# Kernel optimization log

Measured on AMD Instinct MI355X. Metric: run time of the kernel, lower is better.

The kernel has to match this reference:

```python
import jax, jax.numpy as jnp
import numpy as np

EPS = 1e-5
NUM_GROUPS = 32
NUM_HEADS = 4


def setup_inputs() -> dict:
    key = jax.random.key(0)
    ks = jax.random.split(key, 3)
    B, C, H, W = 4, 256, 64, 64
    x = jax.random.normal(ks[0], (B, C, H, W), dtype=jnp.float32)
    gn_w = jnp.ones((C,), jnp.float32)
    gn_b = jnp.zeros((C,), jnp.float32)
    qkv_w = jax.random.normal(ks[1], (3 * C, C), dtype=jnp.float32) * (C ** -0.5)
    qkv_b = jnp.zeros((3 * C,), jnp.float32)
    proj_w = jax.random.normal(ks[2], (C, C), dtype=jnp.float32) * (C ** -0.5)
    proj_b = jnp.zeros((C,), jnp.float32)
    return {"x": x, "gn_w": gn_w, "gn_b": gn_b, "qkv_w": qkv_w,
            "qkv_b": qkv_b, "proj_w": proj_w, "proj_b": proj_b}


def _group_norm(x, w, b):
    B, C, H, W = x.shape
    xg = x.reshape(B, NUM_GROUPS, C // NUM_GROUPS, H, W)
    mean = xg.mean(axis=(2, 3, 4), keepdims=True)
    var = xg.var(axis=(2, 3, 4), keepdims=True)
    xn = ((xg - mean) * jax.lax.rsqrt(var + EPS)).reshape(B, C, H, W)
    return xn * w[None, :, None, None] + b[None, :, None, None]


def reference(x, gn_w, gn_b, qkv_w, qkv_b, proj_w, proj_b):
    B, C, H, W = x.shape
    nh = NUM_HEADS
    d = C // nh
    L = H * W
    h = _group_norm(x, gn_w, gn_b)
    # 1x1 conv == channel matmul
    qkv = jnp.einsum('oc,bchw->bohw', qkv_w, h) + qkv_b[None, :, None, None]
    q, k, v = jnp.split(qkv, 3, axis=1)
    # (B, C, H, W) -> (B, nh, L, d)
    def to_heads(t):
        return t.reshape(B, nh, d, L).transpose(0, 1, 3, 2)
    q, k, v = to_heads(q), to_heads(k), to_heads(v)
    scale = d ** -0.5
    attn = jax.nn.softmax(jnp.einsum('bhqd,bhkd->bhqk', q, k) * scale, axis=-1)
    o = jnp.einsum('bhqk,bhkd->bhqd', attn, v)          # (B, nh, L, d)
    o = o.transpose(0, 1, 3, 2).reshape(B, C, H, W)
    o = jnp.einsum('oc,bchw->bohw', proj_w, o) + proj_b[None, :, None, None]
    return x + o
```

## Files before the change

kernel.cpp:

```cpp
#include <hip/hip_runtime.h>

#define B_   4
#define C_   256
#define L_   4096
#define NH_  4
#define D_   64
#define G_   32
#define CPG_ 8

typedef __bf16 bf16x8 __attribute__((ext_vector_type(8)));
typedef float  f32x4  __attribute__((ext_vector_type(4)));

__device__ __forceinline__ ushort f2bf(float f) {
  union { float f; unsigned u; } c; c.f = f;
  unsigned u = c.u;
  return (ushort)((u + 0x7fffu + ((u >> 16) & 1u)) >> 16);
}
__device__ __forceinline__ float bf2f(ushort h) {
  union { unsigned u; float f; } c; c.u = ((unsigned)h) << 16; return c.f;
}
__device__ __forceinline__ unsigned fbits(float f) {
  union { float f; unsigned u; } c; c.f = f; return c.u;
}
__device__ __forceinline__ float fastexp2(float x) {
#if __has_builtin(__builtin_amdgcn_exp2f)
  return __builtin_amdgcn_exp2f(x);
#else
  return exp2f(x);
#endif
}

__global__ __launch_bounds__(256) void cvt_kernel(const float* __restrict__ wq,
                                                  const float* __restrict__ wp,
                                                  ushort* __restrict__ oq,
                                                  ushort* __restrict__ op,
                                                  float* __restrict__ stats) {
  int t = blockIdx.x * 256 + threadIdx.x;
  if (blockIdx.x == 0) stats[threadIdx.x] = 0.f;
  const int NQ4 = (768 * 256) / 4;
  float4 v;
  if (t < NQ4) {
    v = ((const float4*)wq)[t];
    ((ushort4*)oq)[t] = make_ushort4(f2bf(v.x), f2bf(v.y), f2bf(v.z), f2bf(v.w));
  } else {
    int i = t - NQ4;
    v = ((const float4*)wp)[i];
    ((ushort4*)op)[i] = make_ushort4(f2bf(v.x), f2bf(v.y), f2bf(v.z), f2bf(v.w));
  }
}

__global__ __launch_bounds__(256) void gn_stats(const float* __restrict__ x,
                                                float* __restrict__ stats) {
  int bg = blockIdx.x >> 3, chunk = blockIdx.x & 7;
  int b = bg >> 5, g = bg & 31;
  const float* xg = x + ((size_t)b * C_ + g * CPG_) * L_ + chunk * 512;
  int tid = threadIdx.x;

  float s = 0.f, ss = 0.f;
  for (int c = 0; c < CPG_; ++c) {
    float2 v = ((const float2*)(xg + (size_t)c * L_))[tid];
    s  += v.x + v.y;
    ss += v.x * v.x + v.y * v.y;
  }
  for (int off = 32; off; off >>= 1) { s += __shfl_xor(s, off); ss += __shfl_xor(ss, off); }
  __shared__ float red[8];
  int w = tid >> 6;
  if ((tid & 63) == 0) { red[w] = s; red[4 + w] = ss; }
  __syncthreads();
  if (tid == 0) {
    atomicAdd(&stats[bg * 2],     red[0] + red[1] + red[2] + red[3]);
    atomicAdd(&stats[bg * 2 + 1], red[4] + red[5] + red[6] + red[7]);
  }
}

__global__ __launch_bounds__(256) void gn_apply(const float* __restrict__ x,
                                                const float* __restrict__ gw,
                                                const float* __restrict__ gb,
                                                const float* __restrict__ stats,
                                                ushort* __restrict__ hT) {
  int bg = blockIdx.x >> 3, chunk = blockIdx.x & 7;
  int b = bg >> 5, g = bg & 31;
  const float* xg = x + ((size_t)b * C_ + g * CPG_) * L_;
  int tid = threadIdx.x;

  const float inv_n = 1.0f / (CPG_ * L_);
  float mean = stats[bg * 2] * inv_n;
  float var  = stats[bg * 2 + 1] * inv_n - mean * mean;
  float rstd = rsqrtf(var + 1e-5f);

  float wv[CPG_], bv[CPG_];
  for (int c = 0; c < CPG_; ++c) { wv[c] = gw[g * CPG_ + c]; bv[c] = gb[g * CPG_ + c]; }

  for (int li = 0; li < 2; ++li) {
    int l = chunk * 512 + li * 256 + tid;
    union { ushort s[8]; uint4 u; } o;
    for (int c = 0; c < CPG_; ++c) {
      float v = xg[(size_t)c * L_ + l];
      o.s[c] = f2bf((v - mean) * rstd * wv[c] + bv[c]);
    }
    *(uint4*)(hT + ((size_t)b * L_ + l) * C_ + g * CPG_) = o.u;
  }
}

__global__ __launch_bounds__(256) void qkv_kernel(const ushort* __restrict__ hT,
                                                  const ushort* __restrict__ w,
                                                  const float* __restrict__ bias,
                                                  ushort* __restrict__ q,
                                                  ushort* __restrict__ k,
                                                  ushort* __restrict__ v) {
  int wid  = blockIdx.x * 4 + (threadIdx.x >> 6);
  int lane = threadIdx.x & 63;
  int quad = lane >> 4, col = lane & 15;
  int ot   = wid % 12;
  int rest = wid / 12;
  int lt   = rest & 127;
  int b    = rest >> 7;
  int o0 = ot * 64, l0 = lt * 32;

  const ushort* abase = w  + (size_t)(o0 + col) * C_ + quad * 8;
  const ushort* bbase = hT + ((size_t)b * L_ + l0 + col) * C_ + quad * 8;

  f32x4 acc[4][2];
  for (int i = 0; i < 4; ++i) for (int j = 0; j < 2; ++j)
    acc[i][j] = (f32x4){0.f, 0.f, 0.f, 0.f};

#pragma unroll
  for (int k0 = 0; k0 < C_; k0 += 32) {
    bf16x8 a[4], bb[2];
#pragma unroll
    for (int i = 0; i < 4; ++i) a[i]  = *(const bf16x8*)(abase + (size_t)(i * 16) * C_ + k0);
#pragma unroll
    for (int j = 0; j < 2; ++j) bb[j] = *(const bf16x8*)(bbase + (size_t)(j * 16) * C_ + k0);
#pragma unroll
    for (int i = 0; i < 4; ++i)
#pragma unroll
      for (int j = 0; j < 2; ++j)
        acc[i][j] = __builtin_amdgcn_mfma_f32_16x16x32_bf16(a[i], bb[j], acc[i][j], 0, 0, 0);
  }

  int third = o0 >> 8;
  int hh    = (o0 & 255) >> 6;
  float scale = (third == 0) ? 0.180336880111120f : 1.0f;
#pragma unroll
  for (int i = 0; i < 4; ++i) {
    int oo = o0 + i * 16 + quad * 4;
    int dd = i * 16 + quad * 4;
#pragma unroll
    for (int j = 0; j < 2; ++j) {
      int l = l0 + j * 16 + col;
      ushort pk[4];
      for (int r = 0; r < 4; ++r) pk[r] = f2bf((acc[i][j][r] + bias[oo + r]) * scale);
      if (third < 2) {
        ushort* dst = (third ? k : q) + (((size_t)(b * NH_ + hh) * L_ + l) * D_ + dd);
        *(ushort4*)dst = make_ushort4(pk[0], pk[1], pk[2], pk[3]);
      } else {
        for (int r = 0; r < 4; ++r)
          v[((size_t)(b * NH_ + hh) * D_ + dd + r) * L_ + l] = pk[r];
      }
    }
  }
}

__global__ __launch_bounds__(128, 2) void attn_kernel(const ushort* __restrict__ q,
                                                      const ushort* __restrict__ k,
                                                      const ushort* __restrict__ v,
                                                      ushort* __restrict__ p0,
                                                      ushort* __restrict__ p1,
                                                      float* __restrict__ psumbuf) {
  __shared__ __align__(16) ushort k_lds[2][64][72];
  __shared__ __align__(16) ushort v_lds[2][64][72];

  int tid   = threadIdx.x;
  int w     = tid >> 6, lane = tid & 63;
  int quad  = lane >> 4, col = lane & 15;
  int bid   = (int)blockIdx.x;
  bid = (bid & 7) * 128 + (bid >> 3);
  int split = bid >> 9;
  int bh    = (bid >> 5) & 15;
  int qblk  = bid & 31;

  const ushort* qp = q + (size_t)bh * L_ * D_;
  const ushort* kp = k + (size_t)bh * L_ * D_;
  const ushort* vp = v + (size_t)bh * D_ * L_;

  int qrow0 = qblk * 128 + w * 64;
  bf16x8 bq[4][2];
#pragma unroll
  for (int f = 0; f < 4; ++f)
#pragma unroll
    for (int c = 0; c < 2; ++c)
      bq[f][c] = *(const bf16x8*)(qp + (size_t)(qrow0 + f * 16 + col) * D_ + c * 32 + quad * 8);

  f32x4 oacc[4][4];
#pragma unroll
  for (int f = 0; f < 4; ++f)
    for (int t = 0; t < 4; ++t) oacc[f][t] = (f32x4){0.f, 0.f, 0.f, 0.f};
  float psum[4] = {0.f, 0.f, 0.f, 0.f};
  const f32x4 Z = (f32x4){0.f, 0.f, 0.f, 0.f};

  int vrow = tid >> 1, vhalf = tid & 1;
  int kt0 = split * (L_ / 2), kt_end = kt0 + L_ / 2;

#define STAGE_K(NB, A0, A1, A2, A3) { \
    *(uint4*)&k_lds[NB][(tid >> 3)][(tid & 7) * 8]      = A0; \
    *(uint4*)&k_lds[NB][16 + (tid >> 3)][(tid & 7) * 8] = A1; \
    *(uint4*)&k_lds[NB][32 + (tid >> 3)][(tid & 7) * 8] = A2; \
    *(uint4*)&k_lds[NB][48 + (tid >> 3)][(tid & 7) * 8] = A3; \
  }
#define STAGE_V(NB, C0, C1, C2, C3) { \
    ushort* vb_ = &v_lds[NB][vrow][vhalf * 32]; \
    *(uint2*)(vb_ + 0)  = make_uint2(C0.x, C0.y); \
    *(uint2*)(vb_ + 8)  = make_uint2(C0.z, C0.w); \
    *(uint2*)(vb_ + 16) = make_uint2(C1.x, C1.y); \
    *(uint2*)(vb_ + 24) = make_uint2(C1.z, C1.w); \
    *(uint2*)(vb_ + 4)  = make_uint2(C2.x, C2.y); \
    *(uint2*)(vb_ + 12) = make_uint2(C2.z, C2.w); \
    *(uint2*)(vb_ + 20) = make_uint2(C3.x, C3.y); \
    *(uint2*)(vb_ + 28) = make_uint2(C3.z, C3.w); \
  }

  {
    const uint4* ksrc = (const uint4*)(kp + (size_t)kt0 * D_);
    uint4 a0 = ksrc[tid], a1 = ksrc[tid + 128], a2 = ksrc[tid + 256], a3 = ksrc[tid + 384];
    const uint4* vsrc = (const uint4*)(vp + (size_t)vrow * L_ + kt0);
    uint4 c0 = vsrc[vhalf * 4], c1 = vsrc[vhalf * 4 + 1];
    uint4 c2 = vsrc[vhalf * 4 + 2], c3 = vsrc[vhalf * 4 + 3];
    STAGE_K(0, a0, a1, a2, a3);
    STAGE_V(0, c0, c1, c2, c3);
  }
  __syncthreads();

  int cur = 0;
  for (int kt = kt0; kt < kt_end; kt += 64) {
    bool has_next = (kt + 64) < kt_end;

    f32x4 s[2][4][2];
#pragma unroll
    for (int h = 0; h < 2; ++h) {
      bf16x8 a00 = *(const bf16x8*)&k_lds[cur][h * 32 + col][quad * 8];
      bf16x8 a01 = *(const bf16x8*)&k_lds[cur][h * 32 + col][32 + quad * 8];
      bf16x8 a10 = *(const bf16x8*)&k_lds[cur][h * 32 + 16 + col][quad * 8];
      bf16x8 a11 = *(const bf16x8*)&k_lds[cur][h * 32 + 16 + col][32 + quad * 8];
#pragma unroll
      for (int f = 0; f < 4; ++f) {
        s[h][f][0] = __builtin_amdgcn_mfma_f32_16x16x32_bf16(a00, bq[f][0], Z, 0, 0, 0);
        s[h][f][1] = __builtin_amdgcn_mfma_f32_16x16x32_bf16(a10, bq[f][0], Z, 0, 0, 0);
        s[h][f][0] = __builtin_amdgcn_mfma_f32_16x16x32_bf16(a01, bq[f][1], s[h][f][0], 0, 0, 0);
        s[h][f][1] = __builtin_amdgcn_mfma_f32_16x16x32_bf16(a11, bq[f][1], s[h][f][1], 0, 0, 0);
      }
    }

    uint4 nk0, nk1, nk2, nk3, nv0, nv1, nv2, nv3;
    if (has_next) {
      const uint4* ksrc = (const uint4*)(kp + (size_t)(kt + 64) * D_);
      nk0 = ksrc[tid]; nk1 = ksrc[tid + 128]; nk2 = ksrc[tid + 256]; nk3 = ksrc[tid + 384];
      const uint4* vsrc = (const uint4*)(vp + (size_t)vrow * L_ + (kt + 64));
      nv0 = vsrc[vhalf * 4];     nv1 = vsrc[vhalf * 4 + 1];
      nv2 = vsrc[vhalf * 4 + 2]; nv3 = vsrc[vhalf * 4 + 3];
    }

#pragma unroll
    for (int h = 0; h < 2; ++h) {
      bf16x8 pb[4];
#pragma unroll
      for (int f = 0; f < 4; ++f) {
        float pe0[4], pe1[4];
#pragma unroll
        for (int r = 0; r < 4; ++r) {
          pe0[r] = fastexp2(s[h][f][0][r]);
          pe1[r] = fastexp2(s[h][f][1][r]);
        }
        psum[f] += ((pe0[0] + pe0[1]) + (pe0[2] + pe0[3])) +
                   ((pe1[0] + pe1[1]) + (pe1[2] + pe1[3]));
        union { unsigned u[4]; bf16x8 v8; } pc;
        pc.u[0] = __builtin_amdgcn_perm(fbits(pe0[1]), fbits(pe0[0]), 0x07060302u);
        pc.u[1] = __builtin_amdgcn_perm(fbits(pe0[3]), fbits(pe0[2]), 0x07060302u);
        pc.u[2] = __builtin_amdgcn_perm(fbits(pe1[1]), fbits(pe1[0]), 0x07060302u);
        pc.u[3] = __builtin_amdgcn_perm(fbits(pe1[3]), fbits(pe1[2]), 0x07060302u);
        pb[f] = pc.v8;
      }
#pragma unroll
      for (int t = 0; t < 4; ++t) {
        bf16x8 av = *(const bf16x8*)&v_lds[cur][t * 16 + col][h * 32 + quad * 8];
#pragma unroll
        for (int f = 0; f < 4; ++f)
          oacc[f][t] = __builtin_amdgcn_mfma_f32_16x16x32_bf16(av, pb[f], oacc[f][t], 0, 0, 0);
      }
    }

    if (has_next) {
      int nb = cur ^ 1;
      STAGE_K(nb, nk0, nk1, nk2, nk3);
      STAGE_V(nb, nv0, nv1, nv2, nv3);
      __syncthreads();
      cur = nb;
    }
  }
#undef STAGE_K
#undef STAGE_V

  ushort* po = split ? p1 : p0;
#pragma unroll
  for (int f = 0; f < 4; ++f) {
    psum[f] += __shfl_xor(psum[f], 16);
    psum[f] += __shfl_xor(psum[f], 32);
    for (int t = 0; t < 4; ++t) {
      ushort ok[4];
      for (int r = 0; r < 4; ++r) ok[r] = f2bf(oacc[f][t][r]);
      ushort* dst = po + ((size_t)bh * L_ + qrow0 + f * 16 + col) * D_ + t * 16 + quad * 4;
      *(ushort4*)dst = make_ushort4(ok[0], ok[1], ok[2], ok[3]);
    }
    if (quad == 0)
      psumbuf[split * (16 * L_) + bh * L_ + qrow0 + f * 16 + col] = psum[f];
  }
}

__global__ __launch_bounds__(256) void comb_kernel(ushort* __restrict__ p0,
                                                   const ushort* __restrict__ p1,
                                                   const float* __restrict__ ps) {
  int idx = blockIdx.x * 256 + threadIdx.x;
  int row = idx >> 4;
  float inv = 1.0f / (ps[row] + ps[16 * L_ + row]);
  ushort4 a = ((const ushort4*)p0)[idx];
  ushort4 b = ((const ushort4*)p1)[idx];
  ((ushort4*)p0)[idx] = make_ushort4(
      f2bf((bf2f(a.x) + bf2f(b.x)) * inv),
      f2bf((bf2f(a.y) + bf2f(b.y)) * inv),
      f2bf((bf2f(a.z) + bf2f(b.z)) * inv),
      f2bf((bf2f(a.w) + bf2f(b.w)) * inv));
}

__global__ __launch_bounds__(256) void proj_kernel(const ushort* __restrict__ oin,
                                                   const ushort* __restrict__ pw,
                                                   const float* __restrict__ pb,
                                                   const float* __restrict__ x,
                                                   float* __restrict__ out) {
  int wid  = blockIdx.x * 4 + (threadIdx.x >> 6);
  int lane = threadIdx.x & 63;
  int quad = lane >> 4, col = lane & 15;
  int oct  = wid & 7;
  int rest = wid >> 3;
  int lt   = rest & 127;
  int b    = rest >> 7;
  int l0 = lt * 32, oc0 = oct * 32;

  f32x4 acc[2][2];
  for (int i = 0; i < 2; ++i) for (int j = 0; j < 2; ++j)
    acc[i][j] = (f32x4){0.f, 0.f, 0.f, 0.f};

#pragma unroll
  for (int k0 = 0; k0 < C_; k0 += 32) {
    int hh = k0 >> 6, dk = k0 & 63;
    bf16x8 a[2], bb[2];
#pragma unroll
    for (int i = 0; i < 2; ++i)
      a[i] = *(const bf16x8*)(oin + ((size_t)(b * NH_ + hh) * L_ + l0 + i * 16 + col) * D_ + dk + quad * 8);
#pragma unroll
    for (int j = 0; j < 2; ++j)
      bb[j] = *(const bf16x8*)(pw + (size_t)(oc0 + j * 16 + col) * C_ + k0 + quad * 8);
#pragma unroll
    for (int i = 0; i < 2; ++i)
#pragma unroll
      for (int j = 0; j < 2; ++j)
        acc[i][j] = __builtin_amdgcn_mfma_f32_16x16x32_bf16(a[i], bb[j], acc[i][j], 0, 0, 0);
  }

#pragma unroll
  for (int j = 0; j < 2; ++j) {
    int oc = oc0 + j * 16 + col;
    float bias = pb[oc];
#pragma unroll
    for (int i = 0; i < 2; ++i) {
      int l = l0 + i * 16 + quad * 4;
      size_t off = ((size_t)b * C_ + oc) * L_ + l;
      float4 xv = *(const float4*)(x + off);
      float4 ov = make_float4(acc[i][j][0] + bias + xv.x,
                              acc[i][j][1] + bias + xv.y,
                              acc[i][j][2] + bias + xv.z,
                              acc[i][j][3] + bias + xv.w);
      *(float4*)(out + off) = ov;
    }
  }
}

extern "C" void kernel_launch(void* const* d_in, const int* in_sizes, int n_in,
                              void* d_out, int out_size, void* d_ws, size_t ws_size,
                              hipStream_t stream) {
  const float* x      = (const float*)d_in[0];
  const float* gn_w   = (const float*)d_in[1];
  const float* gn_b   = (const float*)d_in[2];
  const float* qkv_w  = (const float*)d_in[3];
  const float* qkv_b  = (const float*)d_in[4];
  const float* proj_w = (const float*)d_in[5];
  const float* proj_b = (const float*)d_in[6];
  float* out = (float*)d_out;

  const size_t TEN = (size_t)B_ * C_ * L_;
  ushort* ws  = (ushort*)d_ws;
  ushort* q   = ws;
  ushort* k   = ws + TEN;
  ushort* v   = ws + 2 * TEN;
  ushort* oat = ws + 3 * TEN;
  ushort* wq  = ws + 4 * TEN;
  ushort* wp  = wq + 768 * 256;
  float*  stats = (float*)(wp + 256 * 256);
  ushort* hT  = (ushort*)d_out;
  ushort* p1  = (ushort*)d_out + TEN;
  float*  psb = (float*)d_out;

  cvt_kernel <<<256,       256, 0, stream>>>(qkv_w, proj_w, wq, wp, stats);
  gn_stats   <<<1024,      256, 0, stream>>>(x, stats);
  gn_apply   <<<1024,      256, 0, stream>>>(x, gn_w, gn_b, stats, hT);
  qkv_kernel <<<6144 / 4,  256, 0, stream>>>(hT, wq, qkv_b, q, k, v);
  attn_kernel<<<1024,      128, 0, stream>>>(q, k, v, oat, p1, psb);
  comb_kernel<<<4096,      256, 0, stream>>>(oat, p1, psb);
  proj_kernel<<<4096 / 4,  256, 0, stream>>>(oat, wp, proj_b, x, out);
}
```

Measured before the change: 224.4 us.

## Halve attention query tile, load V directly from global, swizzle K LDS

The attention kernel now gives each block 64 query rows instead of 128 (32 per wave), which doubles the grid to 2048 blocks and raises the launch-bounds occupancy hint from 2 to 3. V is no longer staged in shared memory: each wave reads its V fragments straight from global memory inside the loop. K uses an unpadded 64-wide LDS tile with an XOR swizzle to avoid bank conflicts, and the next K tile's prefetch is issued before the QK MFMAs. The goal is higher occupancy and less LDS traffic. The trade-off is that each block reuses K/V across half as many queries, so global and L2 traffic for K and V roughly doubles, and the V loads are narrow 8-byte accesses that sit in the critical path.

```diff
diff --git a/kernel.cpp b/kernel.cpp
--- a/kernel.cpp
+++ b/kernel.cpp
@@ -161,72 +161,60 @@
   }
 }
 
-__global__ __launch_bounds__(128, 2) void attn_kernel(const ushort* __restrict__ q,
+__global__ __launch_bounds__(128, 3) void attn_kernel(const ushort* __restrict__ q,
                                                       const ushort* __restrict__ k,
                                                       const ushort* __restrict__ v,
                                                       ushort* __restrict__ p0,
                                                       ushort* __restrict__ p1,
                                                       float* __restrict__ psumbuf) {
-  __shared__ __align__(16) ushort k_lds[2][64][72];
-  __shared__ __align__(16) ushort v_lds[2][64][72];
+  __shared__ __align__(16) ushort k_lds[2][64][64];
 
   int tid   = threadIdx.x;
   int w     = tid >> 6, lane = tid & 63;
   int quad  = lane >> 4, col = lane & 15;
   int bid   = (int)blockIdx.x;
-  bid = (bid & 7) * 128 + (bid >> 3);
-  int split = bid >> 9;
-  int bh    = (bid >> 5) & 15;
-  int qblk  = bid & 31;
+  bid = (bid & 7) * 256 + (bid >> 3);
+  int split = bid >> 10;
+  int bh    = (bid >> 6) & 15;
+  int qblk  = bid & 63;
 
   const ushort* qp = q + (size_t)bh * L_ * D_;
   const ushort* kp = k + (size_t)bh * L_ * D_;
   const ushort* vp = v + (size_t)bh * D_ * L_;
 
-  int qrow0 = qblk * 128 + w * 64;
-  bf16x8 bq[4][2];
-#pragma unroll
-  for (int f = 0; f < 4; ++f)
+  int qrow0 = qblk * 64 + w * 32;
+  bf16x8 bq[2][2];
+#pragma unroll
+  for (int f = 0; f < 2; ++f)
 #pragma unroll
     for (int c = 0; c < 2; ++c)
       bq[f][c] = *(const bf16x8*)(qp + (size_t)(qrow0 + f * 16 + col) * D_ + c * 32 + quad * 8);
 
-  f32x4 oacc[4][4];
-#pragma unroll
-  for (int f = 0; f < 4; ++f)
+  f32x4 oacc[2][4];
+#pragma unroll
+  for (int f = 0; f < 2; ++f)
     for (int t = 0; t < 4; ++t) oacc[f][t] = (f32x4){0.f, 0.f, 0.f, 0.f};
-  float psum[4] = {0.f, 0.f, 0.f, 0.f};
+  float psum[2] = {0.f, 0.f};
   const f32x4 Z = (f32x4){0.f, 0.f, 0.f, 0.f};
 
-  int vrow = tid >> 1, vhalf = tid & 1;
+  int wrow = tid >> 3;
+  int winn = ((tid & 7) ^ (wrow & 7)) * 8;
+  int sw0 = ((quad)     ^ (col & 7)) * 8;
+  int sw4 = ((quad + 4) ^ (col & 7)) * 8;
+
   int kt0 = split * (L_ / 2), kt_end = kt0 + L_ / 2;
 
 #define STAGE_K(NB, A0, A1, A2, A3) { \
-    *(uint4*)&k_lds[NB][(tid >> 3)][(tid & 7) * 8]      = A0; \
-    *(uint4*)&k_lds[NB][16 + (tid >> 3)][(tid & 7) * 8] = A1; \
-    *(uint4*)&k_lds[NB][32 + (tid >> 3)][(tid & 7) * 8] = A2; \
-    *(uint4*)&k_lds[NB][48 + (tid >> 3)][(tid & 7) * 8] = A3; \
-  }
-#define STAGE_V(NB, C0, C1, C2, C3) { \
-    ushort* vb_ = &v_lds[NB][vrow][vhalf * 32]; \
-    *(uint2*)(vb_ + 0)  = make_uint2(C0.x, C0.y); \
-    *(uint2*)(vb_ + 8)  = make_uint2(C0.z, C0.w); \
-    *(uint2*)(vb_ + 16) = make_uint2(C1.x, C1.y); \
-    *(uint2*)(vb_ + 24) = make_uint2(C1.z, C1.w); \
-    *(uint2*)(vb_ + 4)  = make_uint2(C2.x, C2.y); \
-    *(uint2*)(vb_ + 12) = make_uint2(C2.z, C2.w); \
-    *(uint2*)(vb_ + 20) = make_uint2(C3.x, C3.y); \
-    *(uint2*)(vb_ + 28) = make_uint2(C3.z, C3.w); \
+    *(uint4*)&k_lds[NB][wrow][winn]      = A0; \
+    *(uint4*)&k_lds[NB][16 + wrow][winn] = A1; \
+    *(uint4*)&k_lds[NB][32 + wrow][winn] = A2; \
+    *(uint4*)&k_lds[NB][48 + wrow][winn] = A3; \
   }
 
   {
     const uint4* ksrc = (const uint4*)(kp + (size_t)kt0 * D_);
     uint4 a0 = ksrc[tid], a1 = ksrc[tid + 128], a2 = ksrc[tid + 256], a3 = ksrc[tid + 384];
-    const uint4* vsrc = (const uint4*)(vp + (size_t)vrow * L_ + kt0);
-    uint4 c0 = vsrc[vhalf * 4], c1 = vsrc[vhalf * 4 + 1];
-    uint4 c2 = vsrc[vhalf * 4 + 2], c3 = vsrc[vhalf * 4 + 3];
     STAGE_K(0, a0, a1, a2, a3);
-    STAGE_V(0, c0, c1, c2, c3);
   }
   __syncthreads();
 
@@ -234,15 +222,21 @@
   for (int kt = kt0; kt < kt_end; kt += 64) {
     bool has_next = (kt + 64) < kt_end;
 
-    f32x4 s[2][4][2];
+    uint4 nk0, nk1, nk2, nk3;
+    if (has_next) {
+      const uint4* ksrc = (const uint4*)(kp + (size_t)(kt + 64) * D_);
+      nk0 = ksrc[tid]; nk1 = ksrc[tid + 128]; nk2 = ksrc[tid + 256]; nk3 = ksrc[tid + 384];
+    }
+
+    f32x4 s[2][2][2];
 #pragma unroll
     for (int h = 0; h < 2; ++h) {
-      bf16x8 a00 = *(const bf16x8*)&k_lds[cur][h * 32 + col][quad * 8];
-      bf16x8 a01 = *(const bf16x8*)&k_lds[cur][h * 32 + col][32 + quad * 8];
-      bf16x8 a10 = *(const bf16x8*)&k_lds[cur][h * 32 + 16 + col][quad * 8];
-      bf16x8 a11 = *(const bf16x8*)&k_lds[cur][h * 32 + 16 + col][32 + quad * 8];
-#pragma unroll
-      for (int f = 0; f < 4; ++f) {
+      bf16x8 a00 = *(const bf16x8*)&k_lds[cur][h * 32 + col][sw0];
+      bf16x8 a01 = *(const bf16x8*)&k_lds[cur][h * 32 + col][sw4];
+      bf16x8 a10 = *(const bf16x8*)&k_lds[cur][h * 32 + 16 + col][sw0];
+      bf16x8 a11 = *(const bf16x8*)&k_lds[cur][h * 32 + 16 + col][sw4];
+#pragma unroll
+      for (int f = 0; f < 2; ++f) {
         s[h][f][0] = __builtin_amdgcn_mfma_f32_16x16x32_bf16(a00, bq[f][0], Z, 0, 0, 0);
         s[h][f][1] = __builtin_amdgcn_mfma_f32_16x16x32_bf16(a10, bq[f][0], Z, 0, 0, 0);
         s[h][f][0] = __builtin_amdgcn_mfma_f32_16x16x32_bf16(a01, bq[f][1], s[h][f][0], 0, 0, 0);
@@ -250,20 +244,19 @@
       }
     }
 
-    uint4 nk0, nk1, nk2, nk3, nv0, nv1, nv2, nv3;
-    if (has_next) {
-      const uint4* ksrc = (const uint4*)(kp + (size_t)(kt + 64) * D_);
-      nk0 = ksrc[tid]; nk1 = ksrc[tid + 128]; nk2 = ksrc[tid + 256]; nk3 = ksrc[tid + 384];
-      const uint4* vsrc = (const uint4*)(vp + (size_t)vrow * L_ + (kt + 64));
-      nv0 = vsrc[vhalf * 4];     nv1 = vsrc[vhalf * 4 + 1];
-      nv2 = vsrc[vhalf * 4 + 2]; nv3 = vsrc[vhalf * 4 + 3];
-    }
-
 #pragma unroll
     for (int h = 0; h < 2; ++h) {
-      bf16x8 pb[4];
-#pragma unroll
-      for (int f = 0; f < 4; ++f) {
+      uint2 vf[4][2];
+#pragma unroll
+      for (int t = 0; t < 4; ++t) {
+        const ushort* vb = vp + (size_t)(t * 16 + col) * L_ + kt + h * 32 + quad * 4;
+        vf[t][0] = *(const uint2*)vb;
+        vf[t][1] = *(const uint2*)(vb + 16);
+      }
+
+      bf16x8 pb[2];
+#pragma unroll
+      for (int f = 0; f < 2; ++f) {
         float pe0[4], pe1[4];
 #pragma unroll
         for (int r = 0; r < 4; ++r) {
@@ -281,27 +274,27 @@
       }
 #pragma unroll
       for (int t = 0; t < 4; ++t) {
-        bf16x8 av = *(const bf16x8*)&v_lds[cur][t * 16 + col][h * 32 + quad * 8];
-#pragma unroll
-        for (int f = 0; f < 4; ++f)
-          oacc[f][t] = __builtin_amdgcn_mfma_f32_16x16x32_bf16(av, pb[f], oacc[f][t], 0, 0, 0);
+        union { uint2 u2[2]; bf16x8 v8; } vc;
+        vc.u2[0] = vf[t][0];
+        vc.u2[1] = vf[t][1];
+#pragma unroll
+        for (int f = 0; f < 2; ++f)
+          oacc[f][t] = __builtin_amdgcn_mfma_f32_16x16x32_bf16(vc.v8, pb[f], oacc[f][t], 0, 0, 0);
       }
     }
 
     if (has_next) {
       int nb = cur ^ 1;
       STAGE_K(nb, nk0, nk1, nk2, nk3);
-      STAGE_V(nb, nv0, nv1, nv2, nv3);
       __syncthreads();
       cur = nb;
     }
   }
 #undef STAGE_K
-#undef STAGE_V
 
   ushort* po = split ? p1 : p0;
 #pragma unroll
-  for (int f = 0; f < 4; ++f) {
+  for (int f = 0; f < 2; ++f) {
     psum[f] += __shfl_xor(psum[f], 16);
     psum[f] += __shfl_xor(psum[f], 32);
     for (int t = 0; t < 4; ++t) {
@@ -412,7 +405,7 @@
   gn_stats   <<<1024,      256, 0, stream>>>(x, stats);
   gn_apply   <<<1024,      256, 0, stream>>>(x, gn_w, gn_b, stats, hT);
   qkv_kernel <<<6144 / 4,  256, 0, stream>>>(hT, wq, qkv_b, q, k, v);
-  attn_kernel<<<1024,      128, 0, stream>>>(q, k, v, oat, p1, psb);
+  attn_kernel<<<2048,      128, 0, stream>>>(q, k, v, oat, p1, psb);
   comb_kernel<<<4096,      256, 0, stream>>>(oat, p1, psb);
   proj_kernel<<<4096 / 4,  256, 0, stream>>>(oat, wp, proj_b, x, out);
 }
```

Measured after the change: 452.2 us. 102% more time.
